# Kernel optimization log

Hardware: AMD Instinct MI355X
Metric: run time of the kernel (lower is better)

The kernel has to match this reference:

```python
import jax, jax.numpy as jnp
import numpy as np

NGRID, NLAYER = 8192, 24
NPERIODS, NOBS, NC = 50, 4096, 200
SIGMA = 1.0
VREF = 3.0          # reference crustal Vs (km/s) for depth-sensitivity scale
RAYLEIGH_FACTOR = 0.92


def setup_inputs() -> dict:
    key = jax.random.key(0)
    k1, k2, k3 = jax.random.split(key, 3)
    # S-wave velocity model, 2.0-4.0 km/s, flattened as in log_prob(Vs_flat)
    Vs_flat = (2.0 + 2.0 * jax.random.uniform(k1, (NGRID, NLAYER))).reshape(-1).astype(jnp.float32)
    # Ray-path averaging matrix: nonnegative, rows sum to 1 (slowness average)
    A = jax.random.uniform(k2, (NOBS, NGRID), dtype=jnp.float32)
    A = A / A.sum(axis=1, keepdims=True)
    # Beamforming energy spectra per observation pair: (Nobs, Nperiods, Nc)
    energy = jax.random.uniform(k3, (NOBS, NPERIODS, NC), dtype=jnp.float32)
    # Monotone phase-velocity axis per observation: (Nobs, Nc)
    c_axis = jnp.zeros((NOBS, NC), jnp.float32) + jnp.linspace(1.5, 5.0, NC, dtype=jnp.float32)
    thick = jnp.full((NLAYER,), 2.0, jnp.float32)          # 2 km layers
    periods = jnp.linspace(1.0, 60.0, NPERIODS, dtype=jnp.float32)
    return {"Vs_flat": Vs_flat, "A": A, "energy": energy, "c_axis": c_axis,
            "thick": thick, "periods": periods}


def _dispersion_all_cells(Vs, thick, periods):
    # Differentiable surrogate for the batched surf96 forward across all grid cells.
    # Vs: (G, L), thick: (L,), periods: (P,)  ->  c_true: (G, P)
    z = jnp.cumsum(thick) - 0.5 * thick                      # layer-center depths (L,)
    depth_scale = VREF * periods / 3.0                       # ~ sensing depth per period (P,)
    w = jnp.exp(-z[None, :] / depth_scale[:, None]) * thick[None, :]  # (P, L)
    w = w / w.sum(axis=1, keepdims=True)
    return RAYLEIGH_FACTOR * jnp.einsum('pl,gl->gp', w, Vs)  # (G, P)


def reference(Vs_flat, A, energy, c_axis, thick, periods):
    Vs = Vs_flat.reshape(NGRID, NLAYER)
    c_true = _dispersion_all_cells(Vs, thick, periods)       # (Ngrid, Nperiods)
    # _apply_A: slowness averaging along ray paths
    s_pred = A @ (1.0 / c_true)                              # (Nobs, Nperiods)
    c_pred = 1.0 / s_pred
    # _interp1d_torch, vectorized over all (obs, period) pairs
    idx = jax.vmap(jnp.searchsorted)(c_axis, c_pred)         # (Nobs, Nperiods)
    idx = jnp.clip(idx, 1, NC - 1)
    c0 = jnp.take_along_axis(c_axis, idx - 1, axis=1)
    c1 = jnp.take_along_axis(c_axis, idx, axis=1)
    e0 = jnp.take_along_axis(energy, (idx - 1)[:, :, None], axis=2)[..., 0]
    e1 = jnp.take_along_axis(energy, idx[:, :, None], axis=2)[..., 0]
    w = (c_pred - c0) / (c1 - c0 + 1e-12)
    e_interp = e0 + w * (e1 - e0)
    e_max = energy.max(axis=-1)                              # (Nobs, Nperiods)
    log_like = -jnp.sum(e_max - e_interp) / (SIGMA ** 2)
    return log_like
```

## Files before the change

### kernel.cpp

```cpp
#include <hip/hip_runtime.h>

#define NGRID 8192
#define NLAYER 24
#define NPERIODS 50
#define NOBS 4096
#define NC 200
#define PP 64
#define NSPLIT 16
#define WPB 4
#define GC (NGRID / (NSPLIT * WPB))
#define KG 32
#define ASTR 36
#define NBINS 1024
#define OTILE 64
#define VREF 3.0f

__global__ __launch_bounds__(256) void k1_rpad(const float* __restrict__ Vs,
                                               const float* __restrict__ thick,
                                               const float* __restrict__ periods,
                                               float* __restrict__ r_pad,
                                               float* __restrict__ bins) {
    __shared__ float w_sh[NLAYER][NPERIODS];
    __shared__ float z_sh[NLAYER];
    int tid = threadIdx.x;
    if (blockIdx.x == 0) {
        for (int i = tid; i < NBINS; i += 256) bins[i] = 0.f;
    }
    if (tid < NLAYER) {
        float c = 0.f;
        for (int i = 0; i <= tid; ++i) c += thick[i];
        z_sh[tid] = c - 0.5f * thick[tid];
    }
    __syncthreads();
    if (tid < NPERIODS) {
        float ds = (VREF / 3.0f) * periods[tid];
        float tmp[NLAYER];
        float s = 0.f;
        #pragma unroll
        for (int l = 0; l < NLAYER; ++l) {
            float v = expf(-z_sh[l] / ds) * thick[l];
            tmp[l] = v; s += v;
        }
        float inv = 1.f / s;
        #pragma unroll
        for (int l = 0; l < NLAYER; ++l) w_sh[l][tid] = tmp[l] * inv;
    }
    __syncthreads();
    int idx = blockIdx.x * 256 + tid;
    int g = idx >> 6, p = idx & 63;
    float r = 0.f;
    if (p < NPERIODS) {
        const float4* vp = (const float4*)(Vs + (size_t)g * NLAYER);
        float s = 0.f;
        #pragma unroll
        for (int q = 0; q < NLAYER / 4; ++q) {
            float4 t = vp[q];
            s = fmaf(w_sh[4*q+0][p], t.x, s);
            s = fmaf(w_sh[4*q+1][p], t.y, s);
            s = fmaf(w_sh[4*q+2][p], t.z, s);
            s = fmaf(w_sh[4*q+3][p], t.w, s);
        }
        r = 1.0f / (0.92f * s);
    }
    r_pad[idx] = r;
}

__global__ __launch_bounds__(256) void k2_gemm(const float* __restrict__ A,
                                               const float* __restrict__ r_pad,
                                               float* __restrict__ partial) {
    __shared__ float lds[WPB * OTILE * ASTR];
    int tid  = threadIdx.x;
    int lane = tid & 63;
    int wv   = __builtin_amdgcn_readfirstlane(tid >> 6);
    int o_base = blockIdx.x * OTILE;
    int split  = blockIdx.y;
    float* Aw = lds + wv * (OTILE * ASTR);

    float acc[NPERIODS];
    #pragma unroll
    for (int p = 0; p < NPERIODS; ++p) acc[p] = 0.f;

    int g_wave = (split * WPB + wv) * GC;

    #pragma unroll 1
    for (int kt = 0; kt < GC / KG; ++kt) {
        int g0 = g_wave + kt * KG;
        #pragma unroll
        for (int s = 0; s < 8; ++s) {
            int f   = s * 64 + lane;
            int row = f >> 3;
            int c4  = (f & 7) * 4;
            float4 t = *(const float4*)(A + (size_t)(o_base + row) * NGRID + g0 + c4);
            *(float4*)(Aw + row * ASTR + c4) = t;
        }
        #pragma unroll 1
        for (int gg = 0; gg < KG; gg += 4) {
            float4 a4 = *(const float4*)(Aw + lane * ASTR + gg);
            const float* rr = r_pad + (size_t)(g0 + gg) * PP;
            #pragma unroll
            for (int j = 0; j < 4; ++j) {
                float aj = (j == 0) ? a4.x : (j == 1) ? a4.y : (j == 2) ? a4.z : a4.w;
                const float* rj = rr + j * PP;
                #pragma unroll
                for (int p = 0; p < NPERIODS; ++p) acc[p] = fmaf(aj, rj[p], acc[p]);
            }
        }
    }

    float* outp = partial + (size_t)split * (NOBS * NPERIODS) + (size_t)o_base * NPERIODS;
    #pragma unroll 1
    for (int h = 0; h < 4; ++h) {
        __syncthreads();
        float* rw = lds + wv * (OTILE * 17);
        #pragma unroll
        for (int q = 0; q < 16; ++q) {
            int p = h * 16 + q;
            rw[lane * 17 + q] = (p < NPERIODS) ? acc[p] : 0.f;
        }
        __syncthreads();
        for (int e = tid; e < OTILE * 16; e += 256) {
            int oo = e >> 4, q = e & 15;
            int p  = h * 16 + q;
            if (p < NPERIODS) {
                float v = 0.f;
                #pragma unroll
                for (int w2 = 0; w2 < WPB; ++w2) v += lds[w2 * (OTILE * 17) + oo * 17 + q];
                outp[oo * NPERIODS + p] = v;
            }
        }
    }
}

__global__ __launch_bounds__(256) void k2b_reduce(const float* __restrict__ partial,
                                                  float* __restrict__ cpred) {
    int idx = blockIdx.x * 256 + threadIdx.x;
    int o = idx >> 6, p = idx & 63;
    float v = 0.f;
    if (p < NPERIODS) {
        float s = 0.f;
        #pragma unroll
        for (int sp = 0; sp < NSPLIT; ++sp)
            s += partial[(size_t)sp * (NOBS * NPERIODS) + (size_t)o * NPERIODS + p];
        v = 1.0f / s;
    }
    cpred[idx] = v;
}

__global__ __launch_bounds__(256) void k3_main(const float* __restrict__ energy,
                                               const float* __restrict__ c_axis,
                                               const float* __restrict__ cpred,
                                               float* __restrict__ bins) {
    __shared__ float csh[NC];
    __shared__ float red[4];
    int tid  = threadIdx.x;
    int lane = tid & 63;
    int wv   = tid >> 6;
    int o    = blockIdx.x;

    if (tid < NC) csh[tid] = c_axis[(size_t)o * NC + tid];
    __syncthreads();

    bool act = lane < NC / 4;
    float4 ca = act ? *(const float4*)(csh + 4 * lane) : make_float4(9e30f, 9e30f, 9e30f, 9e30f);
    const float* ebase = energy + (size_t)o * NPERIODS * NC;
    float local = 0.f;

    for (int p0 = wv; p0 < NPERIODS; p0 += 8) {
        int p1 = p0 + 4;
        bool has1 = p1 < NPERIODS;
        int p1c = has1 ? p1 : p0;
        float cpA = cpred[(size_t)o * PP + p0];
        float cpB = cpred[(size_t)o * PP + p1c];
        const float* erA = ebase + (size_t)p0 * NC;
        const float* erB = ebase + (size_t)p1c * NC;
        float4 eA = act ? *(const float4*)(erA + 4 * lane) : make_float4(-1e30f, -1e30f, -1e30f, -1e30f);
        float4 eB = act ? *(const float4*)(erB + 4 * lane) : make_float4(-1e30f, -1e30f, -1e30f, -1e30f);

        int cntA = __popcll(__ballot(ca.x < cpA)) + __popcll(__ballot(ca.y < cpA))
                 + __popcll(__ballot(ca.z < cpA)) + __popcll(__ballot(ca.w < cpA));
        int cntB = __popcll(__ballot(ca.x < cpB)) + __popcll(__ballot(ca.y < cpB))
                 + __popcll(__ballot(ca.z < cpB)) + __popcll(__ballot(ca.w < cpB));

        float mA = fmaxf(fmaxf(eA.x, eA.y), fmaxf(eA.z, eA.w));
        float mB = fmaxf(fmaxf(eB.x, eB.y), fmaxf(eB.z, eB.w));
        #pragma unroll
        for (int m = 32; m; m >>= 1) {
            mA = fmaxf(mA, __shfl_xor(mA, m, 64));
            mB = fmaxf(mB, __shfl_xor(mB, m, 64));
        }

        int iA = cntA < 1 ? 1 : (cntA > NC - 1 ? NC - 1 : cntA);
        int iB = cntB < 1 ? 1 : (cntB > NC - 1 ? NC - 1 : cntB);

        int a0 = iA - 1, a1 = iA, b0 = iB - 1, b1 = iB;
        float sA0 = ((a0 & 3) == 0) ? eA.x : ((a0 & 3) == 1) ? eA.y : ((a0 & 3) == 2) ? eA.z : eA.w;
        float sA1 = ((a1 & 3) == 0) ? eA.x : ((a1 & 3) == 1) ? eA.y : ((a1 & 3) == 2) ? eA.z : eA.w;
        float sB0 = ((b0 & 3) == 0) ? eB.x : ((b0 & 3) == 1) ? eB.y : ((b0 & 3) == 2) ? eB.z : eB.w;
        float sB1 = ((b1 & 3) == 0) ? eB.x : ((b1 & 3) == 1) ? eB.y : ((b1 & 3) == 2) ? eB.z : eB.w;
        float e0A = __shfl(sA0, a0 >> 2, 64), e1A = __shfl(sA1, a1 >> 2, 64);
        float e0B = __shfl(sB0, b0 >> 2, 64), e1B = __shfl(sB1, b1 >> 2, 64);

        float c0A = csh[a0], c1A = csh[a1];
        float c0B = csh[b0], c1B = csh[b1];
        float wA = (cpA - c0A) / (c1A - c0A + 1e-12f);
        float wB = (cpB - c0B) / (c1B - c0B + 1e-12f);
        float eiA = fmaf(wA, e1A - e0A, e0A);
        float eiB = fmaf(wB, e1B - e0B, e0B);
        local += mA - eiA;
        local += has1 ? (mB - eiB) : 0.f;
    }
    if (lane == 0) red[wv] = local;
    __syncthreads();
    if (tid == 0)
        atomicAdd(&bins[blockIdx.x & (NBINS - 1)], red[0] + red[1] + red[2] + red[3]);
}

__global__ __launch_bounds__(256) void k4_final(const float* __restrict__ bins,
                                                float* __restrict__ out) {
    __shared__ float red[4];
    int tid = threadIdx.x;
    float s = 0.f;
    for (int i = tid; i < NBINS; i += 256) s += bins[i];
    #pragma unroll
    for (int m = 32; m; m >>= 1) s += __shfl_xor(s, m, 64);
    int lane = tid & 63, wv = tid >> 6;
    if (lane == 0) red[wv] = s;
    __syncthreads();
    if (tid == 0) out[0] = -(red[0] + red[1] + red[2] + red[3]);
}

extern "C" void kernel_launch(void* const* d_in, const int* in_sizes, int n_in,
                              void* d_out, int out_size, void* d_ws, size_t ws_size,
                              hipStream_t stream) {
    const float* Vs      = (const float*)d_in[0];
    const float* A       = (const float*)d_in[1];
    const float* energy  = (const float*)d_in[2];
    const float* c_axis  = (const float*)d_in[3];
    const float* thick   = (const float*)d_in[4];
    const float* periods = (const float*)d_in[5];
    float* out = (float*)d_out;

    float* ws      = (float*)d_ws;
    float* r_pad   = ws;
    float* partial = r_pad + (size_t)NGRID * PP;
    float* cpred   = partial + (size_t)NSPLIT * NOBS * NPERIODS;
    float* bins    = cpred + (size_t)NOBS * PP;

    hipLaunchKernelGGL(k1_rpad, dim3((NGRID * 64) / 256), dim3(256), 0, stream,
                       Vs, thick, periods, r_pad, bins);
    hipLaunchKernelGGL(k2_gemm, dim3(NOBS / OTILE, NSPLIT), dim3(256), 0, stream,
                       A, r_pad, partial);
    hipLaunchKernelGGL(k2b_reduce, dim3((NOBS * 64) / 256), dim3(256), 0, stream,
                       partial, cpred);
    hipLaunchKernelGGL(k3_main, dim3(NOBS), dim3(256), 0, stream,
                       energy, c_axis, cpred, bins);
    hipLaunchKernelGGL(k4_final, dim3(1), dim3(256), 0, stream, bins, out);
}
```

Baseline: 389.6 us.

## Split GEMM periods across waves sharing one A tile instead of splitting K

```diff
diff --git a/kernel.cpp b/kernel.cpp
--- a/kernel.cpp
+++ b/kernel.cpp
@@ -7,10 +7,10 @@
 #define NC 200
 #define PP 64
 #define NSPLIT 16
-#define WPB 4
-#define GC (NGRID / (NSPLIT * WPB))
+#define GC (NGRID / NSPLIT)
 #define KG 32
 #define ASTR 36
+#define NPW 13
 #define NBINS 1024
 #define OTILE 64
 #define VREF 3.0f
@@ -67,88 +67,70 @@
 
 __global__ __launch_bounds__(256) void k2_gemm(const float* __restrict__ A,
                                                const float* __restrict__ r_pad,
-                                               float* __restrict__ partial) {
-    __shared__ float lds[WPB * OTILE * ASTR];
+                                               float* __restrict__ partial_t) {
+    __shared__ float Aw[OTILE * ASTR];
     int tid  = threadIdx.x;
     int lane = tid & 63;
     int wv   = __builtin_amdgcn_readfirstlane(tid >> 6);
     int o_base = blockIdx.x * OTILE;
     int split  = blockIdx.y;
-    float* Aw = lds + wv * (OTILE * ASTR);
-
-    float acc[NPERIODS];
-    #pragma unroll
-    for (int p = 0; p < NPERIODS; ++p) acc[p] = 0.f;
-
-    int g_wave = (split * WPB + wv) * GC;
+    int pbase  = wv * NPW;
+
+    float acc[NPW];
+    #pragma unroll
+    for (int p = 0; p < NPW; ++p) acc[p] = 0.f;
+
+    int g_blk = split * GC;
 
     #pragma unroll 1
     for (int kt = 0; kt < GC / KG; ++kt) {
-        int g0 = g_wave + kt * KG;
-        #pragma unroll
-        for (int s = 0; s < 8; ++s) {
-            int f   = s * 64 + lane;
+        int g0 = g_blk + kt * KG;
+        __syncthreads();
+        #pragma unroll
+        for (int s = 0; s < 2; ++s) {
+            int f   = s * 256 + tid;
             int row = f >> 3;
             int c4  = (f & 7) * 4;
             float4 t = *(const float4*)(A + (size_t)(o_base + row) * NGRID + g0 + c4);
             *(float4*)(Aw + row * ASTR + c4) = t;
         }
+        __syncthreads();
         #pragma unroll 1
         for (int gg = 0; gg < KG; gg += 4) {
             float4 a4 = *(const float4*)(Aw + lane * ASTR + gg);
-            const float* rr = r_pad + (size_t)(g0 + gg) * PP;
+            const float* rr = r_pad + (size_t)(g0 + gg) * PP + pbase;
             #pragma unroll
             for (int j = 0; j < 4; ++j) {
                 float aj = (j == 0) ? a4.x : (j == 1) ? a4.y : (j == 2) ? a4.z : a4.w;
-                const float* rj = rr + j * PP;
                 #pragma unroll
-                for (int p = 0; p < NPERIODS; ++p) acc[p] = fmaf(aj, rj[p], acc[p]);
+                for (int p = 0; p < NPW; ++p)
+                    acc[p] = fmaf(aj, rr[j * PP + p], acc[p]);
             }
         }
     }
 
-    float* outp = partial + (size_t)split * (NOBS * NPERIODS) + (size_t)o_base * NPERIODS;
-    #pragma unroll 1
-    for (int h = 0; h < 4; ++h) {
-        __syncthreads();
-        float* rw = lds + wv * (OTILE * 17);
-        #pragma unroll
-        for (int q = 0; q < 16; ++q) {
-            int p = h * 16 + q;
-            rw[lane * 17 + q] = (p < NPERIODS) ? acc[p] : 0.f;
-        }
-        __syncthreads();
-        for (int e = tid; e < OTILE * 16; e += 256) {
-            int oo = e >> 4, q = e & 15;
-            int p  = h * 16 + q;
-            if (p < NPERIODS) {
-                float v = 0.f;
-                #pragma unroll
-                for (int w2 = 0; w2 < WPB; ++w2) v += lds[w2 * (OTILE * 17) + oo * 17 + q];
-                outp[oo * NPERIODS + p] = v;
-            }
-        }
-    }
-}
-
-__global__ __launch_bounds__(256) void k2b_reduce(const float* __restrict__ partial,
-                                                  float* __restrict__ cpred) {
+    float* outp = partial_t + (size_t)split * (NPERIODS * NOBS);
+    #pragma unroll
+    for (int p = 0; p < NPW; ++p) {
+        int pp = pbase + p;
+        if (pp < NPERIODS)
+            outp[(size_t)pp * NOBS + o_base + lane] = acc[p];
+    }
+}
+
+__global__ __launch_bounds__(256) void k2b_reduce(const float* __restrict__ partial_t,
+                                                  float* __restrict__ cpred_t) {
     int idx = blockIdx.x * 256 + threadIdx.x;
-    int o = idx >> 6, p = idx & 63;
-    float v = 0.f;
-    if (p < NPERIODS) {
-        float s = 0.f;
-        #pragma unroll
-        for (int sp = 0; sp < NSPLIT; ++sp)
-            s += partial[(size_t)sp * (NOBS * NPERIODS) + (size_t)o * NPERIODS + p];
-        v = 1.0f / s;
-    }
-    cpred[idx] = v;
+    float s = 0.f;
+    #pragma unroll
+    for (int sp = 0; sp < NSPLIT; ++sp)
+        s += partial_t[(size_t)sp * (NPERIODS * NOBS) + idx];
+    cpred_t[idx] = 1.0f / s;
 }
 
 __global__ __launch_bounds__(256) void k3_main(const float* __restrict__ energy,
                                                const float* __restrict__ c_axis,
-                                               const float* __restrict__ cpred,
+                                               const float* __restrict__ cpred_t,
                                                float* __restrict__ bins) {
     __shared__ float csh[NC];
     __shared__ float red[4];
@@ -169,8 +151,8 @@
         int p1 = p0 + 4;
         bool has1 = p1 < NPERIODS;
         int p1c = has1 ? p1 : p0;
-        float cpA = cpred[(size_t)o * PP + p0];
-        float cpB = cpred[(size_t)o * PP + p1c];
+        float cpA = cpred_t[(size_t)p0 * NOBS + o];
+        float cpB = cpred_t[(size_t)p1c * NOBS + o];
         const float* erA = ebase + (size_t)p0 * NC;
         const float* erB = ebase + (size_t)p1c * NC;
         float4 eA = act ? *(const float4*)(erA + 4 * lane) : make_float4(-1e30f, -1e30f, -1e30f, -1e30f);
@@ -240,19 +222,19 @@
     const float* periods = (const float*)d_in[5];
     float* out = (float*)d_out;
 
-    float* ws      = (float*)d_ws;
-    float* r_pad   = ws;
-    float* partial = r_pad + (size_t)NGRID * PP;
-    float* cpred   = partial + (size_t)NSPLIT * NOBS * NPERIODS;
-    float* bins    = cpred + (size_t)NOBS * PP;
+    float* ws        = (float*)d_ws;
+    float* r_pad     = ws;
+    float* partial_t = r_pad + (size_t)NGRID * PP;
+    float* cpred_t   = partial_t + (size_t)NSPLIT * NPERIODS * NOBS;
+    float* bins      = cpred_t + (size_t)NPERIODS * NOBS;
 
     hipLaunchKernelGGL(k1_rpad, dim3((NGRID * 64) / 256), dim3(256), 0, stream,
                        Vs, thick, periods, r_pad, bins);
     hipLaunchKernelGGL(k2_gemm, dim3(NOBS / OTILE, NSPLIT), dim3(256), 0, stream,
-                       A, r_pad, partial);
-    hipLaunchKernelGGL(k2b_reduce, dim3((NOBS * 64) / 256), dim3(256), 0, stream,
-                       partial, cpred);
+                       A, r_pad, partial_t);
+    hipLaunchKernelGGL(k2b_reduce, dim3((NPERIODS * NOBS) / 256), dim3(256), 0, stream,
+                       partial_t, cpred_t);
     hipLaunchKernelGGL(k3_main, dim3(NOBS), dim3(256), 0, stream,
-                       energy, c_axis, cpred, bins);
+                       energy, c_axis, cpred_t, bins);
     hipLaunchKernelGGL(k4_final, dim3(1), dim3(256), 0, stream, bins, out);
 }
```

Result: no change. 391.2 us (+0.4%).
